# Kernel optimization log

Measured on AMD Instinct MI355X. Metric: run time of the kernel, lower is better.

Reference implementation:

```python
import jax, jax.numpy as jnp
import numpy as np

N_T, N_C, N_I = 200000, 100000, 100000  # target / card / ip node counts
E = 300000                               # edges per relation
D, H, OUT = 128, 128, 2                  # embedding_size=in_size, hidden_size, out_size
# etype order: 0 card->target, 1 target->card, 2 ip->target, 3 target->ip


def setup_inputs() -> dict:
    key = jax.random.key(0)
    ks = jax.random.split(key, 14)
    return {
        "x_target": jax.random.normal(ks[0], (N_T, D), jnp.float32),
        "x_card": jax.random.normal(ks[1], (N_C, D), jnp.float32),
        "x_ip": jax.random.normal(ks[2], (N_I, D), jnp.float32),
        "w1": jax.random.normal(ks[3], (4, D, H), jnp.float32) / np.sqrt(D).astype(np.float32),
        "b1": jnp.zeros((4, H), jnp.float32),
        "w2": jax.random.normal(ks[4], (4, H, H), jnp.float32) / np.sqrt(H).astype(np.float32),
        "b2": jnp.zeros((4, H), jnp.float32),
        "w_out": jax.random.normal(ks[5], (H, OUT), jnp.float32) / np.sqrt(H).astype(np.float32),
        "b_out": jnp.zeros((OUT,), jnp.float32),
        "src0": jax.random.randint(ks[6], (E,), 0, N_C, jnp.int32),
        "dst0": jax.random.randint(ks[7], (E,), 0, N_T, jnp.int32),
        "src1": jax.random.randint(ks[8], (E,), 0, N_T, jnp.int32),
        "dst1": jax.random.randint(ks[9], (E,), 0, N_C, jnp.int32),
        "src2": jax.random.randint(ks[10], (E,), 0, N_I, jnp.int32),
        "dst2": jax.random.randint(ks[11], (E,), 0, N_T, jnp.int32),
        "src3": jax.random.randint(ks[12], (E,), 0, N_T, jnp.int32),
        "dst3": jax.random.randint(ks[13], (E,), 0, N_I, jnp.int32),
    }


def _mean_agg(msgs, dst, num_dst):
    # copy_u + mean reduce: segment-sum of gathered messages / in-degree (0 if no edges)
    s = jax.ops.segment_sum(msgs, dst, num_segments=num_dst)
    deg = jax.ops.segment_sum(jnp.ones((msgs.shape[0],), msgs.dtype), dst, num_segments=num_dst)
    return s / jnp.maximum(deg, 1.0)[:, None]


def _hetero_layer(feats, W, B, edges):
    # per-etype Linear on src feats, copy_u/mean per relation, sum across relations per dsttype
    out = {}
    for i, (src, dst, st, dt, nd) in enumerate(edges):
        Wh = feats[st] @ W[i] + B[i]          # [N_src, H] dense GEMM per etype
        agg = _mean_agg(Wh[src], dst, nd)      # gather + segment-mean (irregular)
        out[dt] = agg if dt not in out else out[dt] + agg
    return out


def reference(x_target, x_card, x_ip, w1, b1, w2, b2, w_out, b_out,
              src0, dst0, src1, dst1, src2, dst2, src3, dst3):
    edges = [
        (src0, dst0, "card", "target", N_T),
        (src1, dst1, "target", "card", N_C),
        (src2, dst2, "ip", "target", N_T),
        (src3, dst3, "target", "ip", N_I),
    ]
    h = {"target": x_target, "card": x_card, "ip": x_ip}
    h = _hetero_layer(h, w1, b1, edges)
    h = {k: jax.nn.leaky_relu(v) for k, v in h.items()}  # applied before layer i>0
    h = _hetero_layer(h, w2, b2, edges)
    logits = h["target"] @ w_out + b_out
    return jax.nn.softmax(logits, axis=-1)
```

## Files before the change

### kernel.cpp

```cpp
#include <hip/hip_runtime.h>


#define NT 200000
#define NCARD 100000
#define NIP 100000
#define NE 300000

#define RANGE 8192
#define NCHUNK 8
#define CHUNK 37500
#define CHUNK4 9375
#define RB1 13
#define RB3 13
#define RB0 25
#define RB2 25
#define NB_HISTA ((RB1 + RB3 + RB0 + RB2) * NCHUNK)

typedef __attribute__((ext_vector_type(8))) short s8v;
typedef __attribute__((ext_vector_type(4))) float f4v;

__device__ __forceinline__ unsigned short f2b(float f) {
  unsigned u = __float_as_uint(f);
  u = (u + 0x7fff + ((u >> 16) & 1)) >> 16;
  return (unsigned short)u;
}


__global__ __launch_bounds__(256) void hist_k(
    const int* __restrict__ d1, const int* __restrict__ d3,
    const int* __restrict__ d0, const int* __restrict__ d2,
    int* __restrict__ h1, int* __restrict__ h3,
    int* __restrict__ h0, int* __restrict__ h2,
    int* __restrict__ rk1, int* __restrict__ rk3,
    int* __restrict__ rk0, int* __restrict__ rk2) {
  __shared__ int hsh[RANGE];
  int tid = threadIdx.x;
  int rb = blockIdx.x / NCHUNK, c = blockIdx.x % NCHUNK;
  const int* d; int* hist; int* rkl; int N; int lo;
  if (rb < RB1) { d = d1; hist = h1; rkl = rk1; N = NCARD; lo = rb * RANGE; }
  else if (rb < RB1 + RB3) { d = d3; hist = h3; rkl = rk3; N = NIP; lo = (rb - RB1) * RANGE; }
  else if (rb < RB1 + RB3 + RB0) { d = d0; hist = h0; rkl = rk0; N = NT; lo = (rb - RB1 - RB3) * RANGE; }
  else { d = d2; hist = h2; rkl = rk2; N = NT; lo = (rb - RB1 - RB3 - RB0) * RANGE; }
  int4* h4 = (int4*)hsh;
  for (int b = tid; b < RANGE / 4; b += 256) h4[b] = make_int4(0, 0, 0, 0);
  __syncthreads();
  const int4* d4 = (const int4*)d + (size_t)c * CHUNK4;
  int ebase = c * CHUNK;
  for (int i = tid; i < CHUNK4; i += 256) {
    int4 v = d4[i];
    int e = ebase + i * 4;
    int k0 = v.x - lo, k1 = v.y - lo, k2 = v.z - lo, k3 = v.w - lo;
    if ((unsigned)k0 < (unsigned)RANGE) rkl[e] = atomicAdd(&hsh[k0], 1);
    if ((unsigned)k1 < (unsigned)RANGE) rkl[e + 1] = atomicAdd(&hsh[k1], 1);
    if ((unsigned)k2 < (unsigned)RANGE) rkl[e + 2] = atomicAdd(&hsh[k2], 1);
    if ((unsigned)k3 < (unsigned)RANGE) rkl[e + 3] = atomicAdd(&hsh[k3], 1);
  }
  __syncthreads();
  int n4 = (min(RANGE, N - lo)) >> 2;
  int4* hist4 = (int4*)(hist + (size_t)c * N + lo);
  for (int b = tid; b < n4; b += 256) hist4[b] = h4[b];
}


#define NB_WT 128
#define NB_CVT 12500

__global__ void front_k(const float* __restrict__ x, const float* __restrict__ w1,
                        const float* __restrict__ w2, const float* __restrict__ b2,
                        const float* __restrict__ wout,
                        unsigned short* __restrict__ xb, unsigned short* __restrict__ wtC,
                        unsigned short* __restrict__ wtI, float* __restrict__ wfC,
                        float* __restrict__ wfI, float* __restrict__ bfC,
                        float* __restrict__ bfI) {
  int bid = blockIdx.x, tid = threadIdx.x;
  if (bid < NB_WT) {
    int t = bid * 256 + tid;
    int r = t >> 14;
    int n = (t >> 7) & 127, k = t & 127;
    const float* src = w1 + (r ? 3 : 1) * 16384;
    unsigned short* dst = r ? wtI : wtC;
    dst[n * 128 + k] = f2b(src[k * 128 + n]);
  } else if (bid == NB_WT) {
    int k = tid >> 1, o = tid & 1;
    float sC = 0.f, sI = 0.f;
    for (int j = 0; j < 128; j++) {
      float wo = wout[j * 2 + o];
      sC += w2[0 * 16384 + k * 128 + j] * wo;
      sI += w2[2 * 16384 + k * 128 + j] * wo;
    }
    wfC[k * 2 + o] = sC;
    wfI[k * 2 + o] = sI;
    if (tid < 2) {
      float s = 0.f;
      for (int j = 0; j < 128; j++) s += b2[0 * 128 + j] * wout[j * 2 + tid];
      bfC[tid] = s;
    } else if (tid < 4) {
      int oo = tid - 2;
      float s = 0.f;
      for (int j = 0; j < 128; j++) s += b2[2 * 128 + j] * wout[j * 2 + oo];
      bfI[oo] = s;
    }
  } else {
    long i = (long)(bid - (NB_WT + 1)) * 512 + tid;
    const float4* x4 = (const float4*)x;
    float4 va = x4[i];
    float4 vb = x4[i + 256];
    uint2 oa, ob;
    oa.x = (unsigned)f2b(va.x) | ((unsigned)f2b(va.y) << 16);
    oa.y = (unsigned)f2b(va.z) | ((unsigned)f2b(va.w) << 16);
    ob.x = (unsigned)f2b(vb.x) | ((unsigned)f2b(vb.y) << 16);
    ob.y = (unsigned)f2b(vb.z) | ((unsigned)f2b(vb.w) << 16);
    ((uint2*)xb)[i] = oa;
    ((uint2*)xb)[i + 256] = ob;
  }
}


__global__ void scan1q_k(int* __restrict__ h1, int* __restrict__ deg1,
                         int* __restrict__ off1, int* __restrict__ bs1, int nb1,
                         int* __restrict__ h3, int* __restrict__ deg3,
                         int* __restrict__ off3, int* __restrict__ bs3, int nb3,
                         int* __restrict__ h0, int* __restrict__ deg0,
                         int* __restrict__ off0, int* __restrict__ bs0, int nb0,
                         int* __restrict__ h2, int* __restrict__ deg2,
                         int* __restrict__ off2, int* __restrict__ bs2) {
  __shared__ int s[256];
  int bid = blockIdx.x;
  int* hist; int* deg; int* off; int* bsum; int N; int lb;
  if (bid < nb1) { hist = h1; deg = deg1; off = off1; bsum = bs1; N = NCARD; lb = bid; }
  else if (bid < nb1 + nb3) { hist = h3; deg = deg3; off = off3; bsum = bs3; N = NIP; lb = bid - nb1; }
  else if (bid < nb1 + nb3 + nb0) { hist = h0; deg = deg0; off = off0; bsum = bs0; N = NT; lb = bid - nb1 - nb3; }
  else { hist = h2; deg = deg2; off = off2; bsum = bs2; N = NT; lb = bid - nb1 - nb3 - nb0; }
  int tid = threadIdx.x;
  int i = lb * 256 + tid;
  int v = 0;
  if (i < N) {
    int acc = 0;
#pragma unroll
    for (int c = 0; c < NCHUNK; c++) {
      size_t idx = (size_t)c * N + i;
      int t = hist[idx];
      hist[idx] = acc;
      acc += t;
    }
    deg[i] = acc;
    v = acc;
  }
  s[tid] = v;
  __syncthreads();
  for (int o = 1; o < 256; o <<= 1) {
    int t = (tid >= o) ? s[tid - o] : 0;
    __syncthreads();
    s[tid] += t;
    __syncthreads();
  }
  if (i < N) off[i] = s[tid] - v;
  if (tid == 255) bsum[lb] = s[255];
}

__global__ void scan2q_k(int* __restrict__ bs1, int nb1, int* __restrict__ bs3, int nb3,
                         int* __restrict__ bs0, int nb0, int* __restrict__ bs2, int nb2) {
  __shared__ int s[1024];
  int* bs; int nb;
  if (blockIdx.x == 0) { bs = bs1; nb = nb1; }
  else if (blockIdx.x == 1) { bs = bs3; nb = nb3; }
  else if (blockIdx.x == 2) { bs = bs0; nb = nb0; }
  else { bs = bs2; nb = nb2; }
  int t = threadIdx.x;
  int v = (t < nb) ? bs[t] : 0;
  s[t] = v;
  __syncthreads();
  for (int o = 1; o < 1024; o <<= 1) {
    int u = (t >= o) ? s[t - o] : 0;
    __syncthreads();
    s[t] += u;
    __syncthreads();
  }
  if (t < nb) bs[t] = s[t] - v;
}


#define T4 75000

__global__ void fill4_k(const int* __restrict__ s1, const int* __restrict__ d1,
                        const int* __restrict__ rk1, const int* __restrict__ off1,
                        const int* __restrict__ bs1, const int* __restrict__ h1,
                        int* __restrict__ csr1,
                        const int* __restrict__ s3, const int* __restrict__ d3,
                        const int* __restrict__ rk3, const int* __restrict__ off3,
                        const int* __restrict__ bs3, const int* __restrict__ h3,
                        int* __restrict__ csr3,
                        const int* __restrict__ s0, const int* __restrict__ d0,
                        const int* __restrict__ rk0, const int* __restrict__ off0,
                        const int* __restrict__ bs0, const int* __restrict__ h0,
                        int* __restrict__ csr0,
                        const int* __restrict__ s2, const int* __restrict__ d2,
                        const int* __restrict__ rk2, const int* __restrict__ off2,
                        const int* __restrict__ bs2, const int* __restrict__ h2,
                        int* __restrict__ csr2) {
  int t = blockIdx.x * 256 + threadIdx.x;
  const int* s; const int* d; const int* rk; const int* off; const int* bs;
  const int* h; int* csr; int N; int e4;
  if (t < T4) { s = s1; d = d1; rk = rk1; off = off1; bs = bs1; h = h1; csr = csr1; N = NCARD; e4 = t; }
  else if (t < 2 * T4) { s = s3; d = d3; rk = rk3; off = off3; bs = bs3; h = h3; csr = csr3; N = NIP; e4 = t - T4; }
  else if (t < 3 * T4) { s = s0; d = d0; rk = rk0; off = off0; bs = bs0; h = h0; csr = csr0; N = NT; e4 = t - 2 * T4; }
  else if (t < 4 * T4) { s = s2; d = d2; rk = rk2; off = off2; bs = bs2; h = h2; csr = csr2; N = NT; e4 = t - 3 * T4; }
  else return;
  int4 dv = ((const int4*)d)[e4];
  int4 rv = ((const int4*)rk)[e4];
  int4 sv = ((const int4*)s)[e4];
  int c = e4 / CHUNK4;
  const int* hc = h + (size_t)c * N;
  csr[off[dv.x] + bs[dv.x >> 8] + hc[dv.x] + rv.x] = sv.x;
  csr[off[dv.y] + bs[dv.y >> 8] + hc[dv.y] + rv.y] = sv.y;
  csr[off[dv.z] + bs[dv.z >> 8] + hc[dv.z] + rv.z] = sv.z;
  csr[off[dv.w] + bs[dv.w >> 8] + hc[dv.w] + rv.w] = sv.w;
}


__global__ void aggf_k(const unsigned short* __restrict__ xb,
                       const int* __restrict__ off1, const int* __restrict__ deg1,
                       const int* __restrict__ bs1, const int* __restrict__ csr1,
                       unsigned short* __restrict__ accC,
                       const int* __restrict__ off3, const int* __restrict__ deg3,
                       const int* __restrict__ bs3, const int* __restrict__ csr3,
                       unsigned short* __restrict__ accI) {
  int w = (blockIdx.x * 256 + threadIdx.x) >> 6;
  int lane = threadIdx.x & 63;
  if (w >= NCARD + NIP) return;
  const int* off; const int* deg; const int* bs; const int* csr;
  unsigned short* acc; int row;
  if (w < NCARD) { off = off1; deg = deg1; bs = bs1; csr = csr1; acc = accC; row = w; }
  else { off = off3; deg = deg3; bs = bs3; csr = csr3; acc = accI; row = w - NCARD; }
  int start = off[row] + bs[row >> 8], cnt = deg[row];
  int eg = lane >> 4, fl = lane & 15;
  int cl = cnt < 64 ? cnt : 64;
  int idx = (lane < cl) ? csr[start + lane] : 0;
  float a[8] = {0.f, 0.f, 0.f, 0.f, 0.f, 0.f, 0.f, 0.f};
  for (int i = eg; i < cl; i += 4) {
    int sidx = __shfl(idx, i);
    uint4 v = *(const uint4*)(xb + (size_t)sidx * 128 + fl * 8);
    a[0] += __uint_as_float(v.x << 16);
    a[1] += __uint_as_float(v.x & 0xffff0000u);
    a[2] += __uint_as_float(v.y << 16);
    a[3] += __uint_as_float(v.y & 0xffff0000u);
    a[4] += __uint_as_float(v.z << 16);
    a[5] += __uint_as_float(v.z & 0xffff0000u);
    a[6] += __uint_as_float(v.w << 16);
    a[7] += __uint_as_float(v.w & 0xffff0000u);
  }
  for (int i = 64 + eg; i < cnt; i += 4) {
    int sidx = csr[start + i];
    uint4 v = *(const uint4*)(xb + (size_t)sidx * 128 + fl * 8);
    a[0] += __uint_as_float(v.x << 16);
    a[1] += __uint_as_float(v.x & 0xffff0000u);
    a[2] += __uint_as_float(v.y << 16);
    a[3] += __uint_as_float(v.y & 0xffff0000u);
    a[4] += __uint_as_float(v.z << 16);
    a[5] += __uint_as_float(v.z & 0xffff0000u);
    a[6] += __uint_as_float(v.w << 16);
    a[7] += __uint_as_float(v.w & 0xffff0000u);
  }
#pragma unroll
  for (int j = 0; j < 8; j++) {
    a[j] += __shfl_xor(a[j], 16);
    a[j] += __shfl_xor(a[j], 32);
  }
  if (eg == 0) {
    uint4 o;
    o.x = (unsigned)f2b(a[0]) | ((unsigned)f2b(a[1]) << 16);
    o.y = (unsigned)f2b(a[2]) | ((unsigned)f2b(a[3]) << 16);
    o.z = (unsigned)f2b(a[4]) | ((unsigned)f2b(a[5]) << 16);
    o.w = (unsigned)f2b(a[6]) | ((unsigned)f2b(a[7]) << 16);
    *(uint4*)(acc + (size_t)row * 128 + fl * 8) = o;
  }
}


__global__ __launch_bounds__(256) void gemm_mfma_k(
    const unsigned short* __restrict__ accC, const unsigned short* __restrict__ accI,
    const unsigned short* __restrict__ wtC, const unsigned short* __restrict__ wtI,
    const float* __restrict__ b1, const int* __restrict__ deg1,
    const int* __restrict__ deg3, const float* __restrict__ wfC,
    const float* __restrict__ wfI, const float* __restrict__ bfC,
    const float* __restrict__ bfI, float* __restrict__ zc, float* __restrict__ zi,
    int gbC) {
  int bid = blockIdx.x;
  const unsigned short* accb; const unsigned short* wt; const float* bias;
  const int* deg; const float* wf; const float* bf; float* zout; int M; int lb;
  if (bid < gbC) {
    accb = accC; wt = wtC; bias = b1 + 128; deg = deg1;
    wf = wfC; bf = bfC; zout = zc; M = NCARD; lb = bid;
  } else {
    accb = accI; wt = wtI; bias = b1 + 384; deg = deg3;
    wf = wfI; bf = bfI; zout = zi; M = NIP; lb = bid - gbC;
  }
  int wave = threadIdx.x >> 6, lane = threadIdx.x & 63;
  int q = lane >> 4, cl = lane & 15;
  int r0w = lb * 128 + wave * 32;

  s8v af[2][4];
#pragma unroll
  for (int rt = 0; rt < 2; rt++)
#pragma unroll
    for (int ks = 0; ks < 4; ks++)
      af[rt][ks] = *(const s8v*)(accb + (size_t)(r0w + rt * 16 + cl) * 128 + ks * 32 + q * 8);

  f4v acc[2][8];
#pragma unroll
  for (int rt = 0; rt < 2; rt++)
#pragma unroll
    for (int nt = 0; nt < 8; nt++) acc[rt][nt] = (f4v){0.f, 0.f, 0.f, 0.f};

#pragma unroll
  for (int nt = 0; nt < 8; nt++) {
#pragma unroll
    for (int ks = 0; ks < 4; ks++) {
      s8v bfr = *(const s8v*)(wt + (size_t)(nt * 16 + cl) * 128 + ks * 32 + q * 8);
      acc[0][nt] = __builtin_amdgcn_mfma_f32_16x16x32_bf16(af[0][ks], bfr, acc[0][nt], 0, 0, 0);
      acc[1][nt] = __builtin_amdgcn_mfma_f32_16x16x32_bf16(af[1][ks], bfr, acc[1][nt], 0, 0, 0);
    }
  }

  float2 wfv[8];
  float b1v[8];
#pragma unroll
  for (int nt = 0; nt < 8; nt++) {
    wfv[nt] = ((const float2*)wf)[nt * 16 + cl];
    b1v[nt] = bias[nt * 16 + cl];
  }
  float2 bf2 = *(const float2*)bf;
#pragma unroll
  for (int rt = 0; rt < 2; rt++) {
#pragma unroll
    for (int reg = 0; reg < 4; reg++) {
      int row = r0w + rt * 16 + q * 4 + reg;
      int d = (row < M) ? deg[row] : 0;
      float sc = (d > 0) ? 1.f / (float)d : 0.f;
      float p0 = 0.f, p1 = 0.f;
#pragma unroll
      for (int nt = 0; nt < 8; nt++) {
        float h = 0.f;
        if (d > 0) {
          h = acc[rt][nt][reg] * sc + b1v[nt];
          h = h > 0.f ? h : 0.01f * h;
        }
        p0 += h * wfv[nt].x;
        p1 += h * wfv[nt].y;
      }
#pragma unroll
      for (int o = 1; o < 16; o <<= 1) {
        p0 += __shfl_xor(p0, o);
        p1 += __shfl_xor(p1, o);
      }
      if (cl == 0 && row < M) {
        ((float2*)zout)[row] = make_float2(p0 + bf2.x, p1 + bf2.y);
      }
    }
  }
}


__global__ void finalg_k(const float* __restrict__ zc, const float* __restrict__ zi,
                         const int* __restrict__ off0, const int* __restrict__ deg0,
                         const int* __restrict__ bs0, const int* __restrict__ csr0,
                         const int* __restrict__ off2, const int* __restrict__ deg2,
                         const int* __restrict__ bs2, const int* __restrict__ csr2,
                         const float* __restrict__ bout, float* __restrict__ out) {
  int t = blockIdx.x * 256 + threadIdx.x;
  if (t >= NT) return;
  int d0 = deg0[t], st0 = off0[t] + bs0[t >> 8];
  int d2 = deg2[t], st2 = off2[t] + bs2[t >> 8];
  float l0 = bout[0], l1 = bout[1];
  if (d0 > 0) {
    float ax = 0.f, ay = 0.f;
    for (int i = 0; i < d0; i++) {
      float2 z = ((const float2*)zc)[csr0[st0 + i]];
      ax += z.x; ay += z.y;
    }
    float inv = 1.f / (float)d0;
    l0 += ax * inv; l1 += ay * inv;
  }
  if (d2 > 0) {
    float ax = 0.f, ay = 0.f;
    for (int i = 0; i < d2; i++) {
      float2 z = ((const float2*)zi)[csr2[st2 + i]];
      ax += z.x; ay += z.y;
    }
    float inv = 1.f / (float)d2;
    l0 += ax * inv; l1 += ay * inv;
  }
  float m = fmaxf(l0, l1);
  float e0 = expf(l0 - m), e1 = expf(l1 - m);
  float inv = 1.f / (e0 + e1);
  ((float2*)out)[t] = make_float2(e0 * inv, e1 * inv);
}


extern "C" void kernel_launch(void* const* d_in, const int* in_sizes, int n_in,
                              void* d_out, int out_size, void* d_ws, size_t ws_size,
                              hipStream_t stream) {
  const float* x_target = (const float*)d_in[0];
  const float* w1 = (const float*)d_in[3];
  const float* b1 = (const float*)d_in[4];
  const float* w2 = (const float*)d_in[5];
  const float* b2 = (const float*)d_in[6];
  const float* wout = (const float*)d_in[7];
  const float* bout = (const float*)d_in[8];
  const int* src0 = (const int*)d_in[9];
  const int* dst0 = (const int*)d_in[10];
  const int* src1 = (const int*)d_in[11];
  const int* dst1 = (const int*)d_in[12];
  const int* src2 = (const int*)d_in[13];
  const int* dst2 = (const int*)d_in[14];
  const int* src3 = (const int*)d_in[15];
  const int* dst3 = (const int*)d_in[16];
  float* out = (float*)d_out;

  char* p = (char*)d_ws;
  auto alloc = [&](size_t bytes) -> char* {
    char* r = p;
    p += (bytes + 255) & ~(size_t)255;
    return r;
  };
  int* deg1 = (int*)alloc(NCARD * 4);
  int* deg3 = (int*)alloc(NIP * 4);
  int* deg0 = (int*)alloc(NT * 4);
  int* deg2 = (int*)alloc(NT * 4);
  int* rk1 = (int*)alloc(NE * 4);
  int* rk3 = (int*)alloc(NE * 4);
  int* rk0 = (int*)alloc(NE * 4);
  int* rk2 = (int*)alloc(NE * 4);
  int* off1 = (int*)alloc(NCARD * 4);
  int* off3 = (int*)alloc(NIP * 4);
  int* off0 = (int*)alloc(NT * 4);
  int* off2 = (int*)alloc(NT * 4);
  int* bs1 = (int*)alloc(1024 * 4);
  int* bs3 = (int*)alloc(1024 * 4);
  int* bs0 = (int*)alloc(1024 * 4);
  int* bs2 = (int*)alloc(1024 * 4);
  int* csr1 = (int*)alloc(NE * 4);
  int* csr3 = (int*)alloc(NE * 4);
  int* csr0 = (int*)alloc(NE * 4);
  int* csr2 = (int*)alloc(NE * 4);
  unsigned short* xb = (unsigned short*)alloc((size_t)NT * 128 * 2);
  unsigned short* accC = (unsigned short*)alloc((size_t)NCARD * 128 * 2);
  unsigned short* accI = (unsigned short*)alloc((size_t)NIP * 128 * 2);
  alloc(128 * 128 * 2);
  unsigned short* wtC = (unsigned short*)alloc(16384 * 2);
  unsigned short* wtI = (unsigned short*)alloc(16384 * 2);
  float* zc = (float*)alloc((size_t)NCARD * 2 * 4);
  float* zi = (float*)alloc((size_t)NIP * 2 * 4);
  float* wfC = (float*)alloc(256 * 4);
  float* wfI = (float*)alloc(256 * 4);
  float* bfC = (float*)alloc(2 * 4);
  float* bfI = (float*)alloc(2 * 4);

  int* h1 = (int*)accC;
  int* h3 = h1 + (size_t)NCHUNK * NCARD;
  int* h0 = h3 + (size_t)NCHUNK * NIP;
  int* h2 = h0 + (size_t)NCHUNK * NT;

  hist_k<<<NB_HISTA, 256, 0, stream>>>(dst1, dst3, dst0, dst2, h1, h3, h0, h2,
                                       rk1, rk3, rk0, rk2);

  front_k<<<NB_WT + 1 + NB_CVT, 256, 0, stream>>>(
      x_target, w1, w2, b2, wout, xb, wtC, wtI, wfC, wfI, bfC, bfI);

  int nb1 = (NCARD + 255) / 256, nb3 = (NIP + 255) / 256;
  int nb0 = (NT + 255) / 256, nb2 = (NT + 255) / 256;
  scan1q_k<<<nb1 + nb3 + nb0 + nb2, 256, 0, stream>>>(
      h1, deg1, off1, bs1, nb1, h3, deg3, off3, bs3, nb3,
      h0, deg0, off0, bs0, nb0, h2, deg2, off2, bs2);
  scan2q_k<<<4, 1024, 0, stream>>>(bs1, nb1, bs3, nb3, bs0, nb0, bs2, nb2);

  fill4_k<<<(4 * T4 + 255) / 256, 256, 0, stream>>>(
      src1, dst1, rk1, off1, bs1, h1, csr1, src3, dst3, rk3, off3, bs3, h3, csr3,
      src0, dst0, rk0, off0, bs0, h0, csr0, src2, dst2, rk2, off2, bs2, h2, csr2);

  aggf_k<<<(NCARD + NIP + 3) / 4, 256, 0, stream>>>(
      xb, off1, deg1, bs1, csr1, accC, off3, deg3, bs3, csr3, accI);

  int gbC = (NCARD + 127) / 128, gbI = (NIP + 127) / 128;
  gemm_mfma_k<<<gbC + gbI, 256, 0, stream>>>(accC, accI, wtC, wtI, b1, deg1, deg3,
                                             wfC, wfI, bfC, bfI, zc, zi, gbC);

  finalg_k<<<(NT + 255) / 256, 256, 0, stream>>>(zc, zi, off0, deg0, bs0, csr0,
                                                 off2, deg2, bs2, csr2, bout, out);
}
```

Measured before the change: 412.4 us.

## Fuse neighbor aggregation into MFMA GEMM and drop bf16 conversion of x

Removes the separate pass that converts x_target to bf16 and the standalone aggregation kernel. The GEMM kernel now gathers fp32 neighbor rows directly from x, sums them per destination row, packs the sums to bf16 in LDS and feeds them to MFMA. This avoids writing and re-reading the bf16 copy of x and the aggregate buffers. In exchange, each gathered row is twice as many bytes (fp32), each wave walks its 32 rows serially, and the gather now runs with the occupancy of the GEMM kernel, which uses LDS for the tile. The histogram buffers get their own allocations instead of aliasing the removed aggregate buffer.

```diff
diff --git a/kernel.cpp b/kernel.cpp
--- a/kernel.cpp
+++ b/kernel.cpp
@@ -63,15 +63,13 @@
 
 
 #define NB_WT 128
-#define NB_CVT 12500
-
-__global__ void front_k(const float* __restrict__ x, const float* __restrict__ w1,
+
+__global__ void front_k(const float* __restrict__ w1,
                         const float* __restrict__ w2, const float* __restrict__ b2,
                         const float* __restrict__ wout,
-                        unsigned short* __restrict__ xb, unsigned short* __restrict__ wtC,
-                        unsigned short* __restrict__ wtI, float* __restrict__ wfC,
-                        float* __restrict__ wfI, float* __restrict__ bfC,
-                        float* __restrict__ bfI) {
+                        unsigned short* __restrict__ wtC, unsigned short* __restrict__ wtI,
+                        float* __restrict__ wfC, float* __restrict__ wfI,
+                        float* __restrict__ bfC, float* __restrict__ bfI) {
   int bid = blockIdx.x, tid = threadIdx.x;
   if (bid < NB_WT) {
     int t = bid * 256 + tid;
@@ -80,7 +78,7 @@
     const float* src = w1 + (r ? 3 : 1) * 16384;
     unsigned short* dst = r ? wtI : wtC;
     dst[n * 128 + k] = f2b(src[k * 128 + n]);
-  } else if (bid == NB_WT) {
+  } else {
     int k = tid >> 1, o = tid & 1;
     float sC = 0.f, sI = 0.f;
     for (int j = 0; j < 128; j++) {
@@ -100,18 +98,6 @@
       for (int j = 0; j < 128; j++) s += b2[2 * 128 + j] * wout[j * 2 + oo];
       bfI[oo] = s;
     }
-  } else {
-    long i = (long)(bid - (NB_WT + 1)) * 512 + tid;
-    const float4* x4 = (const float4*)x;
-    float4 va = x4[i];
-    float4 vb = x4[i + 256];
-    uint2 oa, ob;
-    oa.x = (unsigned)f2b(va.x) | ((unsigned)f2b(va.y) << 16);
-    oa.y = (unsigned)f2b(va.z) | ((unsigned)f2b(va.w) << 16);
-    ob.x = (unsigned)f2b(vb.x) | ((unsigned)f2b(vb.y) << 16);
-    ob.y = (unsigned)f2b(vb.z) | ((unsigned)f2b(vb.w) << 16);
-    ((uint2*)xb)[i] = oa;
-    ((uint2*)xb)[i + 256] = ob;
   }
 }
 
@@ -218,93 +204,87 @@
 }
 
 
-__global__ void aggf_k(const unsigned short* __restrict__ xb,
-                       const int* __restrict__ off1, const int* __restrict__ deg1,
-                       const int* __restrict__ bs1, const int* __restrict__ csr1,
-                       unsigned short* __restrict__ accC,
-                       const int* __restrict__ off3, const int* __restrict__ deg3,
-                       const int* __restrict__ bs3, const int* __restrict__ csr3,
-                       unsigned short* __restrict__ accI) {
-  int w = (blockIdx.x * 256 + threadIdx.x) >> 6;
-  int lane = threadIdx.x & 63;
-  if (w >= NCARD + NIP) return;
-  const int* off; const int* deg; const int* bs; const int* csr;
-  unsigned short* acc; int row;
-  if (w < NCARD) { off = off1; deg = deg1; bs = bs1; csr = csr1; acc = accC; row = w; }
-  else { off = off3; deg = deg3; bs = bs3; csr = csr3; acc = accI; row = w - NCARD; }
-  int start = off[row] + bs[row >> 8], cnt = deg[row];
-  int eg = lane >> 4, fl = lane & 15;
-  int cl = cnt < 64 ? cnt : 64;
-  int idx = (lane < cl) ? csr[start + lane] : 0;
-  float a[8] = {0.f, 0.f, 0.f, 0.f, 0.f, 0.f, 0.f, 0.f};
-  for (int i = eg; i < cl; i += 4) {
-    int sidx = __shfl(idx, i);
-    uint4 v = *(const uint4*)(xb + (size_t)sidx * 128 + fl * 8);
-    a[0] += __uint_as_float(v.x << 16);
-    a[1] += __uint_as_float(v.x & 0xffff0000u);
-    a[2] += __uint_as_float(v.y << 16);
-    a[3] += __uint_as_float(v.y & 0xffff0000u);
-    a[4] += __uint_as_float(v.z << 16);
-    a[5] += __uint_as_float(v.z & 0xffff0000u);
-    a[6] += __uint_as_float(v.w << 16);
-    a[7] += __uint_as_float(v.w & 0xffff0000u);
-  }
-  for (int i = 64 + eg; i < cnt; i += 4) {
-    int sidx = csr[start + i];
-    uint4 v = *(const uint4*)(xb + (size_t)sidx * 128 + fl * 8);
-    a[0] += __uint_as_float(v.x << 16);
-    a[1] += __uint_as_float(v.x & 0xffff0000u);
-    a[2] += __uint_as_float(v.y << 16);
-    a[3] += __uint_as_float(v.y & 0xffff0000u);
-    a[4] += __uint_as_float(v.z << 16);
-    a[5] += __uint_as_float(v.z & 0xffff0000u);
-    a[6] += __uint_as_float(v.w << 16);
-    a[7] += __uint_as_float(v.w & 0xffff0000u);
-  }
-#pragma unroll
-  for (int j = 0; j < 8; j++) {
-    a[j] += __shfl_xor(a[j], 16);
-    a[j] += __shfl_xor(a[j], 32);
-  }
-  if (eg == 0) {
-    uint4 o;
-    o.x = (unsigned)f2b(a[0]) | ((unsigned)f2b(a[1]) << 16);
-    o.y = (unsigned)f2b(a[2]) | ((unsigned)f2b(a[3]) << 16);
-    o.z = (unsigned)f2b(a[4]) | ((unsigned)f2b(a[5]) << 16);
-    o.w = (unsigned)f2b(a[6]) | ((unsigned)f2b(a[7]) << 16);
-    *(uint4*)(acc + (size_t)row * 128 + fl * 8) = o;
-  }
-}
-
-
-__global__ __launch_bounds__(256) void gemm_mfma_k(
-    const unsigned short* __restrict__ accC, const unsigned short* __restrict__ accI,
+__global__ __launch_bounds__(256) void gemmfused_k(
+    const float* __restrict__ x,
     const unsigned short* __restrict__ wtC, const unsigned short* __restrict__ wtI,
-    const float* __restrict__ b1, const int* __restrict__ deg1,
-    const int* __restrict__ deg3, const float* __restrict__ wfC,
-    const float* __restrict__ wfI, const float* __restrict__ bfC,
-    const float* __restrict__ bfI, float* __restrict__ zc, float* __restrict__ zi,
-    int gbC) {
+    const float* __restrict__ b1,
+    const int* __restrict__ off1, const int* __restrict__ deg1,
+    const int* __restrict__ bs1, const int* __restrict__ csr1,
+    const int* __restrict__ off3, const int* __restrict__ deg3,
+    const int* __restrict__ bs3, const int* __restrict__ csr3,
+    const float* __restrict__ wfC, const float* __restrict__ wfI,
+    const float* __restrict__ bfC, const float* __restrict__ bfI,
+    float* __restrict__ zc, float* __restrict__ zi, int gbC) {
+  __shared__ unsigned short At[4][32][136];
   int bid = blockIdx.x;
-  const unsigned short* accb; const unsigned short* wt; const float* bias;
-  const int* deg; const float* wf; const float* bf; float* zout; int M; int lb;
+  const unsigned short* wt; const float* bias; const int* off; const int* deg;
+  const int* bs; const int* csr; const float* wf; const float* bf;
+  float* zout; int M; int lb;
   if (bid < gbC) {
-    accb = accC; wt = wtC; bias = b1 + 128; deg = deg1;
+    wt = wtC; bias = b1 + 128; off = off1; deg = deg1; bs = bs1; csr = csr1;
     wf = wfC; bf = bfC; zout = zc; M = NCARD; lb = bid;
   } else {
-    accb = accI; wt = wtI; bias = b1 + 384; deg = deg3;
+    wt = wtI; bias = b1 + 384; off = off3; deg = deg3; bs = bs3; csr = csr3;
     wf = wfI; bf = bfI; zout = zi; M = NIP; lb = bid - gbC;
   }
   int wave = threadIdx.x >> 6, lane = threadIdx.x & 63;
   int q = lane >> 4, cl = lane & 15;
+  int eg = q, fl = cl;
   int r0w = lb * 128 + wave * 32;
 
+  int sv = 0, cv = 0;
+  if (lane < 32) {
+    int rr = r0w + lane;
+    if (rr < M) {
+      sv = off[rr] + bs[rr >> 8];
+      cv = deg[rr];
+    }
+  }
+
+  for (int r = 0; r < 32; r++) {
+    int st = __shfl(sv, r);
+    int cn = __shfl(cv, r);
+    int cl2 = cn < 64 ? cn : 64;
+    int idx = (lane < cl2) ? csr[st + lane] : 0;
+    float a[8] = {0.f, 0.f, 0.f, 0.f, 0.f, 0.f, 0.f, 0.f};
+    for (int i = eg; i < cl2; i += 4) {
+      int sidx = __shfl(idx, i);
+      const float* xr = x + (size_t)sidx * 128 + fl * 8;
+      float4 va = *(const float4*)xr;
+      float4 vb = *(const float4*)(xr + 4);
+      a[0] += va.x; a[1] += va.y; a[2] += va.z; a[3] += va.w;
+      a[4] += vb.x; a[5] += vb.y; a[6] += vb.z; a[7] += vb.w;
+    }
+    for (int i = 64 + eg; i < cn; i += 4) {
+      int sidx = csr[st + i];
+      const float* xr = x + (size_t)sidx * 128 + fl * 8;
+      float4 va = *(const float4*)xr;
+      float4 vb = *(const float4*)(xr + 4);
+      a[0] += va.x; a[1] += va.y; a[2] += va.z; a[3] += va.w;
+      a[4] += vb.x; a[5] += vb.y; a[6] += vb.z; a[7] += vb.w;
+    }
+#pragma unroll
+    for (int j = 0; j < 8; j++) {
+      a[j] += __shfl_xor(a[j], 16);
+      a[j] += __shfl_xor(a[j], 32);
+    }
+    if (eg == 0) {
+      uint4 o;
+      o.x = (unsigned)f2b(a[0]) | ((unsigned)f2b(a[1]) << 16);
+      o.y = (unsigned)f2b(a[2]) | ((unsigned)f2b(a[3]) << 16);
+      o.z = (unsigned)f2b(a[4]) | ((unsigned)f2b(a[5]) << 16);
+      o.w = (unsigned)f2b(a[6]) | ((unsigned)f2b(a[7]) << 16);
+      *(uint4*)&At[wave][r][fl * 8] = o;
+    }
+  }
+  __syncthreads();
+
   s8v af[2][4];
 #pragma unroll
   for (int rt = 0; rt < 2; rt++)
 #pragma unroll
     for (int ks = 0; ks < 4; ks++)
-      af[rt][ks] = *(const s8v*)(accb + (size_t)(r0w + rt * 16 + cl) * 128 + ks * 32 + q * 8);
+      af[rt][ks] = *(const s8v*)&At[wave][rt * 16 + cl][ks * 32 + q * 8];
 
   f4v acc[2][8];
 #pragma unroll
@@ -443,10 +423,10 @@
   int* csr3 = (int*)alloc(NE * 4);
   int* csr0 = (int*)alloc(NE * 4);
   int* csr2 = (int*)alloc(NE * 4);
-  unsigned short* xb = (unsigned short*)alloc((size_t)NT * 128 * 2);
-  unsigned short* accC = (unsigned short*)alloc((size_t)NCARD * 128 * 2);
-  unsigned short* accI = (unsigned short*)alloc((size_t)NIP * 128 * 2);
-  alloc(128 * 128 * 2);
+  int* h1 = (int*)alloc((size_t)NCHUNK * NCARD * 4);
+  int* h3 = (int*)alloc((size_t)NCHUNK * NIP * 4);
+  int* h0 = (int*)alloc((size_t)NCHUNK * NT * 4);
+  int* h2 = (int*)alloc((size_t)NCHUNK * NT * 4);
   unsigned short* wtC = (unsigned short*)alloc(16384 * 2);
   unsigned short* wtI = (unsigned short*)alloc(16384 * 2);
   float* zc = (float*)alloc((size_t)NCARD * 2 * 4);
@@ -456,16 +436,11 @@
   float* bfC = (float*)alloc(2 * 4);
   float* bfI = (float*)alloc(2 * 4);
 
-  int* h1 = (int*)accC;
-  int* h3 = h1 + (size_t)NCHUNK * NCARD;
-  int* h0 = h3 + (size_t)NCHUNK * NIP;
-  int* h2 = h0 + (size_t)NCHUNK * NT;
-
   hist_k<<<NB_HISTA, 256, 0, stream>>>(dst1, dst3, dst0, dst2, h1, h3, h0, h2,
                                        rk1, rk3, rk0, rk2);
 
-  front_k<<<NB_WT + 1 + NB_CVT, 256, 0, stream>>>(
-      x_target, w1, w2, b2, wout, xb, wtC, wtI, wfC, wfI, bfC, bfI);
+  front_k<<<NB_WT + 1, 256, 0, stream>>>(w1, w2, b2, wout, wtC, wtI,
+                                         wfC, wfI, bfC, bfI);
 
   int nb1 = (NCARD + 255) / 256, nb3 = (NIP + 255) / 256;
   int nb0 = (NT + 255) / 256, nb2 = (NT + 255) / 256;
@@ -478,12 +453,10 @@
       src1, dst1, rk1, off1, bs1, h1, csr1, src3, dst3, rk3, off3, bs3, h3, csr3,
       src0, dst0, rk0, off0, bs0, h0, csr0, src2, dst2, rk2, off2, bs2, h2, csr2);
 
-  aggf_k<<<(NCARD + NIP + 3) / 4, 256, 0, stream>>>(
-      xb, off1, deg1, bs1, csr1, accC, off3, deg3, bs3, csr3, accI);
-
   int gbC = (NCARD + 127) / 128, gbI = (NIP + 127) / 128;
-  gemm_mfma_k<<<gbC + gbI, 256, 0, stream>>>(accC, accI, wtC, wtI, b1, deg1, deg3,
-                                             wfC, wfI, bfC, bfI, zc, zi, gbC);
+  gemmfused_k<<<gbC + gbI, 256, 0, stream>>>(
+      x_target, wtC, wtI, b1, off1, deg1, bs1, csr1, off3, deg3, bs3, csr3,
+      wfC, wfI, bfC, bfI, zc, zi, gbC);
 
   finalg_k<<<(NT + 255) / 256, 256, 0, stream>>>(zc, zi, off0, deg0, bs0, csr0,
                                                  off2, deg2, bs2, csr2, bout, out);
```

Result: slower. 439.0 us (+6.4%).
